# Optimization experiments

Hardware: AMD Instinct MI355X
Metric: run time of the kernel (lower is better)

The kernel has to match this reference:

```python
import jax, jax.numpy as jnp
import numpy as np

# ---- config (from init_kwargs) ----
PRE_NMS_THRESH = 0.05
PRE_NMS_TOP_N = 1000
NMS_THRESH = 0.6
FPN_POST_NMS_TOP_N = 100
MIN_SIZE = 0.0
FPN_STRIDES = (8.0, 16.0, 32.0, 64.0, 128.0)
TO_REMOVE = 1.0

M = 2097152   # total FPN points over the batch
N = 16        # images
C = 11        # classes incl. background column (zeroed)


def setup_inputs() -> dict:
    key = jax.random.key(0)
    k1, k2, k3, k4, k5, k6 = jax.random.split(key, 6)
    locations = jax.random.uniform(k1, (M, 2), jnp.float32) * 1024.0
    box_cls = jax.random.normal(k2, (M, C), jnp.float32) * 2.0
    box_regression = jax.random.uniform(k3, (M, 4), jnp.float32) * 4.0
    centerness = jax.random.normal(k4, (M, 1), jnp.float32)
    levels = jax.random.randint(k5, (M,), 0, len(FPN_STRIDES), jnp.int32)
    batch_indices = jnp.sort(jax.random.randint(k6, (M,), 0, N, jnp.int32))
    image_sizes = jnp.tile(jnp.array([[800, 1333]], jnp.int32), (N, 1))  # (h, w)
    return dict(locations=locations, levels=levels, batch_indices=batch_indices,
                box_cls=box_cls, box_regression=box_regression,
                centerness=centerness, image_sizes=image_sizes)


def _iou_matrix(b):
    x1, y1, x2, y2 = b[:, 0], b[:, 1], b[:, 2], b[:, 3]
    area = jnp.clip(x2 - x1 + TO_REMOVE, 0.0) * jnp.clip(y2 - y1 + TO_REMOVE, 0.0)
    xx1 = jnp.maximum(x1[:, None], x1[None, :])
    yy1 = jnp.maximum(y1[:, None], y1[None, :])
    xx2 = jnp.minimum(x2[:, None], x2[None, :])
    yy2 = jnp.minimum(y2[:, None], y2[None, :])
    inter = jnp.clip(xx2 - xx1 + TO_REMOVE, 0.0) * jnp.clip(yy2 - yy1 + TO_REMOVE, 0.0)
    return inter / jnp.maximum(area[:, None] + area[None, :] - inter, 1e-9)


def _greedy_nms(iou, keep0):
    # boxes assumed sorted by descending score; keep0 = validity mask
    K = keep0.shape[0]
    idx = jnp.arange(K)
    def step(keep, i):
        sup = (iou[i] > NMS_THRESH) & (idx > i) & keep[i]
        return keep & ~sup, None
    keep, _ = jax.lax.scan(step, keep0, jnp.arange(K))
    return keep


def _fcos_post(locations, box_cls, box_regression, centerness,
               levels, batch_indices, image_sizes):
    strides = jnp.asarray(FPN_STRIDES, box_regression.dtype)
    reg = box_regression * strides[levels][:, None]          # norm_reg_targets=True
    scores = jax.nn.sigmoid(box_cls) * jax.nn.sigmoid(centerness)  # [M,C]
    scores = scores.at[:, -1].set(0.0)                       # kill background column
    boxes_all = jnp.concatenate([locations - reg[:, :2],
                                 locations + reg[:, 2:]], axis=-1)  # [M,4]

    def per_image(args):
        i, hw = args
        m = (batch_indices == i)[:, None] & (scores > PRE_NMS_THRESH)
        flat = jnp.where(m, scores, 0.0).reshape(-1)          # [M*C]
        topv, topi = jax.lax.top_k(flat, PRE_NMS_TOP_N)       # sorted desc
        pt = topi // C
        cl = (topi % C + 1).astype(jnp.int32)                 # labels = class + 1
        b = boxes_all[pt]                                     # [K,4]
        v0 = topv > 0.0                                       # pad entries -> invalid
        sc = jnp.sqrt(jnp.where(v0, topv, 1.0)) * v0          # sqrt(score), safe at pads
        h = hw[0].astype(b.dtype); w = hw[1].astype(b.dtype)
        x1 = jnp.clip(b[:, 0], 0.0, w - TO_REMOVE)            # clip_to_image
        y1 = jnp.clip(b[:, 1], 0.0, h - TO_REMOVE)
        x2 = jnp.clip(b[:, 2], 0.0, w - TO_REMOVE)
        y2 = jnp.clip(b[:, 3], 0.0, h - TO_REMOVE)
        b = jnp.stack([x1, y1, x2, y2], axis=-1)
        ws = x2 - x1 + TO_REMOVE; hs = y2 - y1 + TO_REMOVE    # remove_small_boxes
        keep0 = v0 & (ws >= MIN_SIZE) & (hs >= MIN_SIZE)
        # class-aware NMS via coordinate offset trick
        max_coord = jnp.max(jnp.where(keep0[:, None], b, 0.0))
        boff = jax.lax.stop_gradient(b + (cl.astype(b.dtype) * (max_coord + 1.0))[:, None])
        keep = _greedy_nms(_iou_matrix(boff), keep0)
        sck = jnp.where(keep, sc, 0.0)
        fv, fi = jax.lax.top_k(sck, FPN_POST_NMS_TOP_N)       # fpn_post_nms_top_n
        return b[fi], fv, cl[fi], fv > 0.0

    boxes_o, scores_o, labels_o, valid_o = jax.lax.map(
        per_image, (jnp.arange(N), image_sizes))
    return boxes_o, scores_o, labels_o, valid_o


def reference(locations, levels, batch_indices, box_cls, box_regression,
              centerness, image_sizes):
    return _fcos_post(locations, box_cls, box_regression, centerness,
                      levels, batch_indices, image_sizes)
```

## Files before the change

kernel.cpp:

```cpp
#include <hip/hip_runtime.h>
#include <math.h>

#pragma clang fp contract(off)

#define MPTS   2097152
#define NIMG   16
#define NCLS   11
#define CUTB   0x3F000000u
#define NB2    1026
#define NB2P   1040
#define MARG   96u
#define CAP    4096
#define SORTN  4096
#define TOPN   1000
#define OUTN   100
#define LCAP   64

typedef unsigned long long u64;

#define SUPW_PER_IMG 8704
__device__ __forceinline__ int chunk_base(int c) {
    return 64 * (16 * c - (c * (c - 1)) / 2);
}

__device__ inline float sigx(float x) {
    float e = (float)exp(-(double)x);
    return 1.0f / (1.0f + e);
}
__device__ inline float sigf(float x) {
    float e = __expf(-x);
    return __builtin_amdgcn_rcpf(1.0f + e);
}
__device__ inline float bfr(float x) {
    unsigned u = __float_as_uint(x);
    unsigned r = (u + 0x7FFFu + ((u >> 16) & 1u)) & 0xFFFF0000u;
    return __uint_as_float(r);
}
__device__ __forceinline__ u64 rdlane64(u64 v, int l) {
    unsigned lo = (unsigned)__builtin_amdgcn_readlane((int)(unsigned)(v & 0xFFFFFFFFull), l);
    unsigned hi = (unsigned)__builtin_amdgcn_readlane((int)(unsigned)(v >> 32), l);
    return ((u64)hi << 32) | (u64)lo;
}

__global__ __launch_bounds__(1024)
void k_hist(const float4* __restrict__ cls4, const float* __restrict__ ctr,
            const int* __restrict__ batch, unsigned* __restrict__ ghist) {
    __shared__ unsigned hist[NB2];
    __shared__ int simg;
    const int F4  = MPTS * NCLS / 4;
    const int FPB = F4 / 512;
    int f0 = blockIdx.x * FPB;
    int t = threadIdx.x;
    for (int i = t; i < NB2; i += 1024) hist[i] = 0;
    if (t == 0) simg = batch[(unsigned)(4u * (unsigned)f0) / NCLS];
    __syncthreads();
    int bi = simg;
    unsigned pc = 0xFFFFFFFFu;
    float sfc = 0.0f;
    int bc = 0;
    for (int f = f0 + t; f < f0 + FPB; f += 1024) {
        float4 v = cls4[f];
        float va[4] = {v.x, v.y, v.z, v.w};
        unsigned e0 = 4u * (unsigned)f;
        #pragma unroll
        for (int j = 0; j < 4; j++) {
            float ck = va[j];
            if (ck <= 0.0f) continue;
            unsigned e = e0 + (unsigned)j;
            unsigned p = e / NCLS;
            unsigned k = e - p * NCLS;
            if (k == 10u) continue;
            if (p != pc) {
                pc = p; sfc = sigf(ctr[p]); bc = batch[p];
            }
            unsigned fb = __float_as_uint(sigf(ck) * sfc);
            if (fb < CUTB) continue;
            unsigned bin = (fb - CUTB) >> 13;
            if (bin >= NB2) bin = NB2 - 1;
            if (bc == bi) atomicAdd(&hist[bin], 1u);
            else          atomicAdd(&ghist[(size_t)bc * NB2P + bin], 1u);
        }
    }
    __syncthreads();
    unsigned* gh = ghist + (size_t)bi * NB2P;
    for (int i = t; i < NB2; i += 1024) {
        unsigned v2 = hist[i];
        if (v2) atomicAdd(&gh[i], v2);
    }
}

__global__ void k_thresh(const unsigned* __restrict__ ghist, unsigned* __restrict__ thrbuf) {
    int img = blockIdx.x;
    const unsigned* h = ghist + (size_t)img * NB2P;
    __shared__ unsigned psum[256];
    int t = threadIdx.x;
    unsigned s = 0;
    int base = t * 5;
    for (int i = 0; i < 5; i++) { int b = base + i; if (b < NB2) s += h[b]; }
    psum[t] = s;
    __syncthreads();
    if (t == 0) {
        unsigned run = 0; int B = 0;
        for (int u = 205; u >= 0; u--) {
            if (run + psum[u] >= (unsigned)TOPN) {
                int btop = u * 5 + 4; if (btop > NB2 - 1) btop = NB2 - 1;
                for (int b = btop; b >= u * 5; b--) {
                    run += h[b];
                    if (run >= (unsigned)TOPN) { B = b; break; }
                }
                break;
            }
            run += psum[u];
        }
        unsigned TB = CUTB + ((unsigned)B << 13) - MARG;
        thrbuf[2 * img] = TB;
        thrbuf[2 * img + 1] = __float_as_uint(__uint_as_float(TB) * 0.998f);
    }
}

__global__ __launch_bounds__(256)
void k_collect(const float4* __restrict__ cls4, const float* __restrict__ ctr,
               const int* __restrict__ batch, const unsigned* __restrict__ thrbuf,
               unsigned* __restrict__ gcnt, unsigned long long* __restrict__ cand) {
    __shared__ unsigned sTB[NIMG];
    __shared__ float sSCR[NIMG];
    __shared__ u64 lbuf[NIMG][LCAP];
    __shared__ unsigned lcnt[NIMG];
    __shared__ unsigned lbase[NIMG];
    int t = threadIdx.x;
    if (t < NIMG) {
        sTB[t]  = thrbuf[2 * t];
        sSCR[t] = __uint_as_float(thrbuf[2 * t + 1]);
        lcnt[t] = 0;
    }
    __syncthreads();
    const int F4  = MPTS * NCLS / 4;
    const int FPB = F4 / 2048;
    int f0 = blockIdx.x * FPB;
    unsigned pc = 0xFFFFFFFFu;
    float cgs = 0.0f, sfc = 0.0f, sxc = 0.0f, scrc = 0.0f;
    bool havex = false;
    int bc = 0; unsigned TBc = 0;
    for (int f = f0 + t; f < f0 + FPB; f += 256) {
        float4 v = cls4[f];
        float va[4] = {v.x, v.y, v.z, v.w};
        unsigned e0 = 4u * (unsigned)f;
        #pragma unroll
        for (int j = 0; j < 4; j++) {
            float ck = va[j];
            if (ck <= -0.001f) continue;
            unsigned e = e0 + (unsigned)j;
            unsigned p = e / NCLS;
            unsigned k = e - p * NCLS;
            if (k == 10u) continue;
            if (p != pc) {
                pc = p; cgs = ctr[p]; bc = batch[p];
                sfc = sigf(cgs); havex = false;
                TBc = sTB[bc]; scrc = sSCR[bc];
            }
            float sf = sigf(ck) * sfc;
            if (sf > scrc) {
                if (!havex) { sxc = sigx(cgs); havex = true; }
                float s = sigx(ck) * sxc;
                unsigned bits = __float_as_uint(s);
                if (bits >= TBc && s > 0.05f) {
                    u64 key = ((u64)bits << 32) | (u64)(0xFFFFFFFFu - e);
                    unsigned slot = atomicAdd(&lcnt[bc], 1u);
                    if (slot < LCAP) lbuf[bc][slot] = key;
                    else {
                        unsigned pos = atomicAdd(&gcnt[bc * 16], 1u);
                        if (pos < CAP) cand[(size_t)bc * CAP + pos] = key;
                    }
                }
            }
        }
    }
    __syncthreads();
    if (t < NIMG) {
        unsigned n = lcnt[t]; if (n > LCAP) n = LCAP;
        lcnt[t] = n;
        lbase[t] = n ? atomicAdd(&gcnt[t * 16], n) : 0u;
    }
    __syncthreads();
    for (int s = t; s < NIMG * LCAP; s += 256) {
        int im = s >> 6;
        int sl = s & (LCAP - 1);
        if (sl < (int)lcnt[im]) {
            unsigned pos = lbase[im] + (unsigned)sl;
            if (pos < CAP) cand[(size_t)im * CAP + pos] = lbuf[im][sl];
        }
    }
}

__global__ __launch_bounds__(1024)
void k_build(const unsigned long long* __restrict__ cand, const unsigned* __restrict__ gcnt,
             const float* __restrict__ loc, const float* __restrict__ breg,
             const int* __restrict__ levels, const int* __restrict__ imsz,
             float* __restrict__ bx, float* __restrict__ sc, int* __restrict__ cl,
             unsigned* __restrict__ k0, float* __restrict__ bo, float* __restrict__ ar) {
    int img = blockIdx.x;
    __shared__ unsigned long long skey[SORTN];
    __shared__ float red[1024];
    __shared__ float smc;
    unsigned n = gcnt[img * 16]; if (n > SORTN) n = SORTN;
    for (int i = threadIdx.x; i < SORTN; i += 1024)
        skey[i] = (i < (int)n) ? cand[(size_t)img * CAP + i] : 0ull;
    __syncthreads();
    for (unsigned kk = 2; kk <= SORTN; kk <<= 1) {
        for (unsigned j = kk >> 1; j > 0; j >>= 1) {
            for (unsigned i = threadIdx.x; i < SORTN; i += 1024) {
                unsigned ixj = i ^ j;
                if (ixj > i) {
                    unsigned long long a = skey[i], b = skey[ixj];
                    bool up = ((i & kk) == 0);
                    bool sw = up ? (a < b) : (a > b);
                    if (sw) { skey[i] = b; skey[ixj] = a; }
                }
            }
            __syncthreads();
        }
    }
    float wmax = (float)imsz[img * 2 + 1] - 1.0f;
    float hmax = (float)imsz[img * 2 + 0] - 1.0f;
    float lmax = 0.0f;
    for (int r = threadIdx.x; r < TOPN; r += 1024) {
        unsigned long long kv = skey[r];
        unsigned bits = (unsigned)(kv >> 32);
        unsigned idx = 0xFFFFFFFFu - (unsigned)(kv & 0xFFFFFFFFull);
        float v = __uint_as_float(bits);
        bool v0 = (kv != 0ull) && (v > 0.0f);
        if (!v0) idx = 0;
        unsigned pt = idx / NCLS;
        int c = (int)(idx - pt * NCLS);
        float lx = loc[(size_t)pt * 2 + 0], ly = loc[(size_t)pt * 2 + 1];
        float st = (float)(8 << levels[pt]);
        float r0 = breg[(size_t)pt * 4 + 0] * st;
        float r1 = breg[(size_t)pt * 4 + 1] * st;
        float r2 = breg[(size_t)pt * 4 + 2] * st;
        float r3 = breg[(size_t)pt * 4 + 3] * st;
        float x1 = lx - r0, y1 = ly - r1, x2 = lx + r2, y2 = ly + r3;
        x1 = fminf(fmaxf(x1, 0.0f), wmax);
        y1 = fminf(fmaxf(y1, 0.0f), hmax);
        x2 = fminf(fmaxf(x2, 0.0f), wmax);
        y2 = fminf(fmaxf(y2, 0.0f), hmax);
        float wss = (x2 - x1) + 1.0f, hss = (y2 - y1) + 1.0f;
        bool keep = v0 && (wss >= 0.0f) && (hss >= 0.0f);
        size_t ob = (size_t)img * TOPN + r;
        bx[ob * 4 + 0] = x1; bx[ob * 4 + 1] = y1;
        bx[ob * 4 + 2] = x2; bx[ob * 4 + 3] = y2;
        sc[ob] = v0 ? sqrtf(v) : 0.0f;
        cl[ob] = c + 1;
        k0[ob] = keep ? 1u : 0u;
        if (keep) lmax = fmaxf(lmax, fmaxf(fmaxf(x1, y1), fmaxf(x2, y2)));
    }
    red[threadIdx.x] = lmax; __syncthreads();
    for (int sft = 512; sft > 0; sft >>= 1) {
        if ((int)threadIdx.x < sft) red[threadIdx.x] = fmaxf(red[threadIdx.x], red[threadIdx.x + sft]);
        __syncthreads();
    }
    if (threadIdx.x == 0) smc = red[0];
    __syncthreads();
    float off1 = smc + 1.0f;
    for (int r = threadIdx.x; r < TOPN; r += 1024) {
        size_t ob = (size_t)img * TOPN + r;
        float o = (float)cl[ob] * off1;
        float x1 = bx[ob * 4 + 0] + o, y1 = bx[ob * 4 + 1] + o;
        float x2 = bx[ob * 4 + 2] + o, y2 = bx[ob * 4 + 3] + o;
        bo[ob * 4 + 0] = x1; bo[ob * 4 + 1] = y1;
        bo[ob * 4 + 2] = x2; bo[ob * 4 + 3] = y2;
        float aw = fmaxf((x2 - x1) + 1.0f, 0.0f);
        float ah = fmaxf((y2 - y1) + 1.0f, 0.0f);
        ar[ob] = aw * ah;
    }
}

__global__ __launch_bounds__(1024)
void k_iou(const float* __restrict__ bo, const float* __restrict__ ar,
           u64* __restrict__ sup) {
    int img = blockIdx.x >> 4;
    int c   = blockIdx.x & 15;
    __shared__ float sx1[1024], sy1[1024], sx2[1024], sy2[1024], sa[1024];
    int tid = threadIdx.x;
    {
        int i = tid;
        if (i < TOPN) {
            size_t ob = (size_t)img * TOPN + i;
            sx1[i] = bo[ob * 4 + 0]; sy1[i] = bo[ob * 4 + 1];
            sx2[i] = bo[ob * 4 + 2]; sy2[i] = bo[ob * 4 + 3];
            sa[i]  = ar[ob];
        } else {
            sx1[i] = 0.0f; sy1[i] = 0.0f; sx2[i] = 0.0f; sy2[i] = 0.0f; sa[i] = 0.0f;
        }
    }
    __syncthreads();
    int width = 16 - c;
    int items = 64 * width;
    u64* supc = sup + (size_t)img * SUPW_PER_IMG + chunk_base(c);
    for (int it = tid; it < items; it += 1024) {
        int r  = it & 63;
        int wq = c + (it >> 6);
        int i  = c * 64 + r;
        if (i >= TOPN) continue;
        float x1 = sx1[i], y1 = sy1[i], x2 = sx2[i], y2 = sy2[i], a = sa[i];
        int j0 = wq * 64;
        u64 m = 0ull;
        #pragma unroll 8
        for (int jj = 0; jj < 64; jj++) {
            int j = j0 + jj;
            float xx1 = fmaxf(x1, sx1[j]);
            float yy1 = fmaxf(y1, sy1[j]);
            float xx2 = fminf(x2, sx2[j]);
            float yy2 = fminf(y2, sy2[j]);
            float iw = fmaxf((xx2 - xx1) + 1.0f, 0.0f);
            float ih = fmaxf((yy2 - yy1) + 1.0f, 0.0f);
            float inter = iw * ih;
            float den = fmaxf((a + sa[j]) - inter, 1e-9f);
            if (inter / den > 0.6f) m |= (1ull << jj);
        }
        u64 vm = ~0ull;
        if (wq == c) vm = (r >= 63) ? 0ull : (~0ull << (r + 1));
        int rem = TOPN - j0;
        if (rem < 64) vm &= (rem <= 0) ? 0ull : ((1ull << rem) - 1ull);
        supc[(size_t)r * width + (wq - c)] = m & vm;
    }
}

__device__ __forceinline__ void scan_pref(const u64* __restrict__ supi, int rg, int w, int t,
                                          int C, u64 (&V)[16], u64 &anyV, u64 &dmy) {
    int wd = 16 - C;
    const u64* rb = supi + chunk_base(C) + (rg << 4) * wd - C + w;
    u64 a = 0ull;
    #pragma unroll
    for (int i = 0; i < 16; i++) {
        u64 x = rb[i * wd];
        V[i] = (w >= C) ? x : 0ull;
        a |= V[i];
    }
    anyV = a;
    dmy = supi[chunk_base(C) + (size_t)t * wd];
}

__device__ __forceinline__ void scan_step(int rg, int w, int C,
                                          u64 (&V)[16], u64 anyV, u64 dmy,
                                          u64 &kw_local) {
    u64 m = rdlane64(kw_local, C);
    u64 act = __ballot(dmy != 0ull) & m;
    while (act) {
        int r = __builtin_ctzll(act);
        u64 d = rdlane64(dmy, r);
        m &= ~d;
        act &= act - 1ull;
        act &= m;
    }
    if (__ballot(anyV != 0ull)) {
        u64 loc = 0ull;
        #pragma unroll
        for (int i = 0; i < 16; i++) {
            int row = (rg << 4) + i;
            loc |= V[i] & ((u64)0 - ((m >> row) & 1ull));
        }
        u64 t1 = loc | __shfl_xor(loc, 16);
        u64 t2 = t1 | __shfl_xor(t1, 32);
        kw_local = ((w == C) ? m : kw_local) & ~t2;
    } else if (w == C) {
        kw_local = m;
    }
}

__global__ __launch_bounds__(64)
void k_scan_out(const u64* __restrict__ sup, const unsigned* __restrict__ k0,
                const float* __restrict__ bx, const float* __restrict__ sc,
                const int* __restrict__ cl, float* __restrict__ out) {
    int img = blockIdx.x;
    int t = threadIdx.x;
    int rg = t >> 4, w = t & 15;
    const u64* supi = sup + (size_t)img * SUPW_PER_IMG;

    u64 kw_local = 0ull;
    #pragma unroll
    for (int q = 0; q < 16; q++) {
        int i = (q << 6) + t;
        unsigned vv = (i < TOPN) ? k0[(size_t)img * TOPN + i] : 0u;
        u64 bal = __ballot(vv != 0u);
        if (w == q) kw_local = bal;
    }

    u64 vA[16], vB[16], anyA, anyB, dA, dB;
    scan_pref(supi, rg, w, t, 0, vA, anyA, dA);
    for (int c = 0; c < 16; c += 2) {
        scan_pref(supi, rg, w, t, c + 1, vB, anyB, dB);
        scan_step(rg, w, c, vA, anyA, dA, kw_local);
        if (c + 2 < 16) scan_pref(supi, rg, w, t, c + 2, vA, anyA, dA);
        scan_step(rg, w, c + 1, vB, anyB, dB, kw_local);
    }

    u64 kws[16];
    #pragma unroll
    for (int q = 0; q < 16; q++) kws[q] = rdlane64(kw_local, q);

    __shared__ int fi[OUTN];
    int total_k = 0;
    #pragma unroll
    for (int q = 0; q < 16; q++) total_k += __popcll(kws[q]);
    int snk = total_k < OUTN ? total_k : OUTN;
    int run = 0;
    #pragma unroll
    for (int q = 0; q < 16; q++) {
        u64 word = kws[q];
        int i = (q << 6) + t;
        int kb = __popcll(word & ((1ull << t) - 1ull));
        bool kept = ((word >> t) & 1ull) != 0ull;
        int krank = run + kb;
        if (kept) {
            if (krank < OUTN) fi[krank] = i;
        } else if (i < TOPN) {
            int slot = snk + (i - krank);
            if (slot < OUTN) fi[slot] = i;
        }
        run += __popcll(word);
    }
    __syncthreads();

    for (int q = t; q < OUTN; q += 64) {
        int r = fi[q];
        bool kv = q < snk;
        size_t ob = (size_t)img * TOPN + r;
        float sv = kv ? sc[ob] : 0.0f;
        int o = img * OUTN + q;
        out[o * 4 + 0] = bfr(bx[ob * 4 + 0]);
        out[o * 4 + 1] = bfr(bx[ob * 4 + 1]);
        out[o * 4 + 2] = bfr(bx[ob * 4 + 2]);
        out[o * 4 + 3] = bfr(bx[ob * 4 + 3]);
        out[6400 + o] = bfr(sv);
        out[8000 + o] = (float)cl[ob];
        out[9600 + o] = (sv > 0.0f) ? 1.0f : 0.0f;
    }
}

extern "C" void kernel_launch(void* const* d_in, const int* in_sizes, int n_in,
                              void* d_out, int out_size, void* d_ws, size_t ws_size,
                              hipStream_t stream) {
    const float* loc    = (const float*)d_in[0];
    const int*   levels = (const int*)d_in[1];
    const int*   batch  = (const int*)d_in[2];
    const float* cls    = (const float*)d_in[3];
    const float* breg   = (const float*)d_in[4];
    const float* ctr    = (const float*)d_in[5];
    const int*   imsz   = (const int*)d_in[6];

    char* ws = (char*)d_ws;
    unsigned long long* cand   = (unsigned long long*)(ws + 0);
    unsigned*           ghist  = (unsigned*)(ws + 524288);
    float*              bx     = (float*)(ws + 852096);
    float*              bo     = (float*)(ws + 1108096);
    float*              ar     = (float*)(ws + 1364096);
    float*              sc     = (float*)(ws + 1428096);
    int*                cl     = (int*)(ws + 1492096);
    unsigned*           k0     = (unsigned*)(ws + 1556096);
    unsigned*           gcnt   = (unsigned*)(ws + 1620096);
    unsigned*           thrbuf = (unsigned*)(ws + 1621120);
    u64*                sup    = (u64*)(ws + 1703936);
    float* out = (float*)d_out;

    hipMemsetAsync(ghist, 0, 16 * NB2P * 4, stream);
    hipMemsetAsync(gcnt, 0, 1024, stream);
    k_hist    <<<512,  1024, 0, stream>>>((const float4*)cls, ctr, batch, ghist);
    k_thresh  <<<16,   256,  0, stream>>>(ghist, thrbuf);
    k_collect <<<2048, 256,  0, stream>>>((const float4*)cls, ctr, batch, thrbuf, gcnt, cand);
    k_build   <<<16,   1024, 0, stream>>>(cand, gcnt, loc, breg, levels, imsz,
                                          bx, sc, cl, k0, bo, ar);
    k_iou     <<<256,  1024, 0, stream>>>(bo, ar, sup);
    k_scan_out<<<16,   64,   0, stream>>>(sup, k0, bx, sc, cl, out);
}
```

Measured before the change: 336.5 us.

## Replace per-image bitonic sort with parallel rank-by-counting top-1000 selection

The single-block-per-image bitonic sort of up to 4096 keys in k_build is replaced by a new k_rank kernel. It spreads each image over 4 blocks, and every candidate computes its rank by comparing against all keys in shared memory, then scatters itself to position rank if that rank is under 1000. This removes the roughly 78 barrier-separated bitonic passes and uses 64 blocks instead of 16, at the cost of O(n^2) comparisons per image. It also adds a memset of the sorted buffer and an extra launch. Keys are unique (they embed the index), so ranks do not collide, and k_build shrinks to 256 threads.

```diff
diff --git a/kernel.cpp b/kernel.cpp
--- a/kernel.cpp
+++ b/kernel.cpp
@@ -11,7 +11,6 @@
 #define NB2P   1040
 #define MARG   96u
 #define CAP    4096
-#define SORTN  4096
 #define TOPN   1000
 #define OUTN   100
 #define LCAP   64
@@ -193,38 +192,45 @@
 }
 
 __global__ __launch_bounds__(1024)
-void k_build(const unsigned long long* __restrict__ cand, const unsigned* __restrict__ gcnt,
+void k_rank(const u64* __restrict__ cand, const unsigned* __restrict__ gcnt,
+            u64* __restrict__ srt) {
+    int img = blockIdx.x >> 2;
+    int sub = blockIdx.x & 3;
+    __shared__ u64 keys[CAP];
+    unsigned n = gcnt[img * 16]; if (n > CAP) n = CAP;
+    for (int i = threadIdx.x; i < (int)n; i += 1024)
+        keys[i] = cand[(size_t)img * CAP + i];
+    __syncthreads();
+    int i = sub * 1024 + (int)threadIdx.x;
+    if (i < (int)n) {
+        u64 me = keys[i];
+        int rank = 0;
+        int j = 0;
+        for (; j + 4 <= (int)n; j += 4) {
+            rank += (keys[j]     > me);
+            rank += (keys[j + 1] > me);
+            rank += (keys[j + 2] > me);
+            rank += (keys[j + 3] > me);
+        }
+        for (; j < (int)n; j++) rank += (keys[j] > me);
+        if (rank < TOPN) srt[(size_t)img * TOPN + rank] = me;
+    }
+}
+
+__global__ __launch_bounds__(256)
+void k_build(const u64* __restrict__ srt,
              const float* __restrict__ loc, const float* __restrict__ breg,
              const int* __restrict__ levels, const int* __restrict__ imsz,
              float* __restrict__ bx, float* __restrict__ sc, int* __restrict__ cl,
              unsigned* __restrict__ k0, float* __restrict__ bo, float* __restrict__ ar) {
     int img = blockIdx.x;
-    __shared__ unsigned long long skey[SORTN];
-    __shared__ float red[1024];
+    __shared__ float red[256];
     __shared__ float smc;
-    unsigned n = gcnt[img * 16]; if (n > SORTN) n = SORTN;
-    for (int i = threadIdx.x; i < SORTN; i += 1024)
-        skey[i] = (i < (int)n) ? cand[(size_t)img * CAP + i] : 0ull;
-    __syncthreads();
-    for (unsigned kk = 2; kk <= SORTN; kk <<= 1) {
-        for (unsigned j = kk >> 1; j > 0; j >>= 1) {
-            for (unsigned i = threadIdx.x; i < SORTN; i += 1024) {
-                unsigned ixj = i ^ j;
-                if (ixj > i) {
-                    unsigned long long a = skey[i], b = skey[ixj];
-                    bool up = ((i & kk) == 0);
-                    bool sw = up ? (a < b) : (a > b);
-                    if (sw) { skey[i] = b; skey[ixj] = a; }
-                }
-            }
-            __syncthreads();
-        }
-    }
     float wmax = (float)imsz[img * 2 + 1] - 1.0f;
     float hmax = (float)imsz[img * 2 + 0] - 1.0f;
     float lmax = 0.0f;
-    for (int r = threadIdx.x; r < TOPN; r += 1024) {
-        unsigned long long kv = skey[r];
+    for (int r = threadIdx.x; r < TOPN; r += 256) {
+        u64 kv = srt[(size_t)img * TOPN + r];
         unsigned bits = (unsigned)(kv >> 32);
         unsigned idx = 0xFFFFFFFFu - (unsigned)(kv & 0xFFFFFFFFull);
         float v = __uint_as_float(bits);
@@ -254,14 +260,14 @@
         if (keep) lmax = fmaxf(lmax, fmaxf(fmaxf(x1, y1), fmaxf(x2, y2)));
     }
     red[threadIdx.x] = lmax; __syncthreads();
-    for (int sft = 512; sft > 0; sft >>= 1) {
+    for (int sft = 128; sft > 0; sft >>= 1) {
         if ((int)threadIdx.x < sft) red[threadIdx.x] = fmaxf(red[threadIdx.x], red[threadIdx.x + sft]);
         __syncthreads();
     }
     if (threadIdx.x == 0) smc = red[0];
     __syncthreads();
     float off1 = smc + 1.0f;
-    for (int r = threadIdx.x; r < TOPN; r += 1024) {
+    for (int r = threadIdx.x; r < TOPN; r += 256) {
         size_t ob = (size_t)img * TOPN + r;
         float o = (float)cl[ob] * off1;
         float x1 = bx[ob * 4 + 0] + o, y1 = bx[ob * 4 + 1] + o;
@@ -451,6 +457,7 @@
     char* ws = (char*)d_ws;
     unsigned long long* cand   = (unsigned long long*)(ws + 0);
     unsigned*           ghist  = (unsigned*)(ws + 524288);
+    u64*                srt    = (u64*)(ws + 591872);
     float*              bx     = (float*)(ws + 852096);
     float*              bo     = (float*)(ws + 1108096);
     float*              ar     = (float*)(ws + 1364096);
@@ -464,10 +471,12 @@
 
     hipMemsetAsync(ghist, 0, 16 * NB2P * 4, stream);
     hipMemsetAsync(gcnt, 0, 1024, stream);
+    hipMemsetAsync(srt, 0, 16 * TOPN * 8, stream);
     k_hist    <<<512,  1024, 0, stream>>>((const float4*)cls, ctr, batch, ghist);
     k_thresh  <<<16,   256,  0, stream>>>(ghist, thrbuf);
     k_collect <<<2048, 256,  0, stream>>>((const float4*)cls, ctr, batch, thrbuf, gcnt, cand);
-    k_build   <<<16,   1024, 0, stream>>>(cand, gcnt, loc, breg, levels, imsz,
+    k_rank    <<<64,   1024, 0, stream>>>(cand, gcnt, srt);
+    k_build   <<<16,   256,  0, stream>>>(srt, loc, breg, levels, imsz,
                                           bx, sc, cl, k0, bo, ar);
     k_iou     <<<256,  1024, 0, stream>>>(bo, ar, sup);
     k_scan_out<<<16,   64,   0, stream>>>(sup, k0, bx, sc, cl, out);
```

Measured after the change: 320.3 us. -4.8%, faster.
